# Optimization experiments

Hardware: AMD Instinct MI355X
Metric: run time of the kernel (lower is better)

## Reference

```python
import jax, jax.numpy as jnp
import numpy as np

B, N, F_IN, F_OUT = 8, 2048, 128, 64
ALPHA = 0.2  # LeakyReLU negative slope
NEG_INF = -9e15


def setup_inputs() -> dict:
    key = jax.random.key(0)
    k1, k2, k3, k4 = jax.random.split(key, 4)
    h = jax.random.normal(k1, (B, N, F_IN), dtype=jnp.float32)
    adj = jax.random.randint(k2, (B, N, N), 0, 2, dtype=jnp.int32)
    # xavier_uniform with gain=1.414 approximated by scaled normals (values are arbitrary params)
    W = jax.random.normal(k3, (F_IN, F_OUT), dtype=jnp.float32) * (1.414 * np.sqrt(2.0 / (F_IN + F_OUT)))
    a = jax.random.normal(k4, (2 * F_OUT, 1), dtype=jnp.float32) * (1.414 * np.sqrt(2.0 / (2 * F_OUT + 1)))
    return {"h": h, "adj": adj, "W": W, "a": a}


def reference(h, adj, W, a):
    # Wh: [B, N, F_out]
    Wh = jnp.einsum('bnf,fo->bno', h, W)
    Fo = W.shape[1]
    a1 = a[:Fo, 0]   # [F_out]
    a2 = a[Fo:, 0]   # [F_out]
    # e[b,i,j] = leakyrelu(Wh[b,i]@a1 + Wh[b,j]@a2)  (== cat(Wh_i,Wh_j)@a, same math, no N^2*2F blowup)
    e1 = jnp.einsum('bno,o->bn', Wh, a1)  # [B, N]
    e2 = jnp.einsum('bno,o->bn', Wh, a2)  # [B, N]
    e = e1[:, :, None] + e2[:, None, :]   # [B, N, N]
    e = jnp.where(e > 0, e, ALPHA * e)    # LeakyReLU
    e = jnp.where(adj > 0, e, NEG_INF)    # mask non-edges
    attention = jax.nn.softmax(e, axis=-1)
    # dropout is identity in inference mode (deterministic reference)
    h_prime = jnp.einsum('bij,bjo->bio', attention, Wh)  # [B, N, F_out]
    return jax.nn.elu(h_prime)  # concat=True branch
```

## Files before the change

### kernel.cpp

```cpp
#include <hip/hip_runtime.h>
#include <hip/hip_bf16.h>

#define BB 8
#define NN 2048
#define FIN 128
#define FO 64
#define ALPHA 0.2f

typedef __attribute__((ext_vector_type(8))) short bf16x8;
typedef __attribute__((ext_vector_type(4))) float f32x4;
typedef __attribute__((ext_vector_type(4))) int i32x4;

typedef __attribute__((address_space(1))) const void gvoid;
typedef __attribute__((address_space(3))) void lvoid;

__device__ inline void gl_lds16(const void* g, void* l) {
    __builtin_amdgcn_global_load_lds((gvoid*)g, (lvoid*)l, 16, 0, 0);
}

__device__ inline short f2bf(float x) {
    unsigned u = __float_as_uint(x);
    u += 0x7fffu + ((u >> 16) & 1u);
    return (short)(u >> 16);
}

__global__ __launch_bounds__(256) void wh_kernel(
    const float* __restrict__ h, const float* __restrict__ W,
    const float* __restrict__ a, float* __restrict__ e1, float* __restrict__ e2,
    float* __restrict__ e2p, short* __restrict__ whF)
{
    const int t  = threadIdx.x;
    const int o  = t & 63;
    const int wv = t >> 6;
    const int r0 = blockIdx.x * 32;
    const float* __restrict__ hrow =
        h + (size_t)(r0 + __builtin_amdgcn_readfirstlane(wv) * 8) * FIN;

    float acc[8];
#pragma unroll
    for (int rr = 0; rr < 8; rr++) acc[rr] = 0.f;

    for (int f = 0; f < FIN; f += 4) {
        const float w0 = W[(f + 0) * FO + o];
        const float w1 = W[(f + 1) * FO + o];
        const float w2 = W[(f + 2) * FO + o];
        const float w3 = W[(f + 3) * FO + o];
#pragma unroll
        for (int rr = 0; rr < 8; rr++) {
            const float4 hv = *(const float4*)(hrow + rr * FIN + f);
            acc[rr] = fmaf(hv.x, w0, acc[rr]);
            acc[rr] = fmaf(hv.y, w1, acc[rr]);
            acc[rr] = fmaf(hv.z, w2, acc[rr]);
            acc[rr] = fmaf(hv.w, w3, acc[rr]);
        }
    }

    const int b   = r0 / NN;
    const int ib0 = r0 - b * NN;
    const int ibb = ib0 + wv * 8;
    const int jc  = ibb >> 5;
    const int qq  = (ibb >> 3) & 3;
    const int ot  = o >> 4, mm = o & 15;
    const int L   = mm + qq * 16;
    bf16x8 frag;
#pragma unroll
    for (int rr = 0; rr < 8; rr++) frag[rr] = f2bf(acc[rr]);
    *(bf16x8*)(whF + ((((size_t)(b * 64 + jc) * 4 + ot) * 64 + L) * 8)) = frag;

    const float a1 = a[o], a2 = a[FO + o];
    float vmax = -3.0e38f;
#pragma unroll
    for (int rr = 0; rr < 8; rr++) {
        float v1 = acc[rr] * a1, v2 = acc[rr] * a2;
#pragma unroll
        for (int msk = 32; msk >= 1; msk >>= 1) {
            v1 += __shfl_xor(v1, msk, 64);
            v2 += __shfl_xor(v2, msk, 64);
        }
        vmax = fmaxf(vmax, v2);
        if (o == 0) { e1[r0 + wv * 8 + rr] = v1; e2[r0 + wv * 8 + rr] = v2; }
    }
    if (o == 0) e2p[b * 256 + (ib0 >> 5) * 4 + wv] = vmax;
}

struct SMemS { int adj[2][16][260]; };
struct SMemC { float comb[4][16][64]; float lsum[4][16]; };
union __align__(16) SMemU { SMemS s; SMemC c; };

__global__ __launch_bounds__(256, 4) void attn_kernel(
    const int* __restrict__ adj, const float* __restrict__ e1,
    const float* __restrict__ e2, const float* __restrict__ e2p,
    const short* __restrict__ whF, float* __restrict__ out)
{
    __shared__ SMemU sm;
    __shared__ float red4[4];
    const int t = threadIdx.x, w = t >> 6, lane = t & 63;
    const int m = lane & 15, q = lane >> 4;
    const int blk = blockIdx.x;
    const int b  = blk >> 7;
    const int i0 = (blk & 127) * 16;
    const int i  = i0 + m;

    float pv = e2p[b * 256 + t];
    const float e1v = e1[b * NN + i];
#pragma unroll
    for (int k = 32; k >= 1; k >>= 1) pv = fmaxf(pv, __shfl_xor(pv, k, 64));
    if (lane == 0) red4[w] = pv;
    __syncthreads();
    const float e2mx = fmaxf(fmaxf(red4[0], red4[1]), fmaxf(red4[2], red4[3]));

    float mi = e1v + e2mx;
    mi = mi > 0.f ? mi : ALPHA * mi;

    const short* whFb = whF + (size_t)b * (64 * 4 * 64 * 8);
    const int* arow0 = adj + ((size_t)(b * NN + i0)) * NN + lane * 4;
    const float* e2b = e2 + b * NN;

    f32x4 acc0 = {0.f,0.f,0.f,0.f}, acc1 = acc0, acc2 = acc0, acc3 = acc0;
    float lsum = 0.f;

#pragma unroll
    for (int k = 0; k < 4; k++)
        gl_lds16(arow0 + (size_t)(w * 4 + k) * NN, &sm.s.adj[0][w * 4 + k][0]);

#pragma unroll 2
    for (int tt = 0; tt < 8; tt++) {
        const int j0 = tt * 256;
        const int cb = tt & 1;

        const short* bfpA = whFb + (size_t)((j0 + w * 64) >> 5) * 2048 + lane * 8;
        bf16x8 b00 = *(const bf16x8*)(bfpA);
        bf16x8 b01 = *(const bf16x8*)(bfpA + 512);
        bf16x8 b02 = *(const bf16x8*)(bfpA + 1024);
        bf16x8 b03 = *(const bf16x8*)(bfpA + 1536);
        const short* bfpB = bfpA + 2048;
        bf16x8 b10 = *(const bf16x8*)(bfpB);
        bf16x8 b11 = *(const bf16x8*)(bfpB + 512);
        bf16x8 b12 = *(const bf16x8*)(bfpB + 1024);
        bf16x8 b13 = *(const bf16x8*)(bfpB + 1536);

        const float* e2w = e2b + j0 + w * 64 + q * 8;
        f32x4 ev00 = *(const f32x4*)(e2w);
        f32x4 ev01 = *(const f32x4*)(e2w + 4);
        f32x4 ev10 = *(const f32x4*)(e2w + 32);
        f32x4 ev11 = *(const f32x4*)(e2w + 36);

        asm volatile("" ::: "memory");

        if (tt < 7) {
            const int jn = j0 + 256;
#pragma unroll
            for (int k = 0; k < 4; k++)
                gl_lds16(arow0 + (size_t)(w * 4 + k) * NN + jn,
                         &sm.s.adj[cb ^ 1][w * 4 + k][0]);
            asm volatile("s_waitcnt vmcnt(16)" ::: "memory");
        } else {
            asm volatile("s_waitcnt vmcnt(12)" ::: "memory");
        }
        __builtin_amdgcn_s_barrier();

#pragma unroll
        for (int s2 = 0; s2 < 2; s2++) {
            const int col = w * 64 + s2 * 32 + q * 8;
            i32x4 a0 = *(const i32x4*)&sm.s.adj[cb][m][col];
            i32x4 a1 = *(const i32x4*)&sm.s.adj[cb][m][col + 4];
            const f32x4 ev0 = s2 ? ev10 : ev00;
            const f32x4 ev1 = s2 ? ev11 : ev01;

            bf16x8 af;
#pragma unroll
            for (int jj = 0; jj < 8; jj++) {
                const int   av  = (jj < 4) ? a0[jj]  : a1[jj - 4];
                const float e2j = (jj < 4) ? ev0[jj] : ev1[jj - 4];
                float e = e1v + e2j;
                e = e > 0.f ? e : ALPHA * e;
                const float pe = (av > 0) ? __expf(e - mi) : 0.f;
                lsum += pe;
                af[jj] = f2bf(pe);
            }

            if (s2 == 0) {
                acc0 = __builtin_amdgcn_mfma_f32_16x16x32_bf16(af, b00, acc0, 0, 0, 0);
                acc1 = __builtin_amdgcn_mfma_f32_16x16x32_bf16(af, b01, acc1, 0, 0, 0);
                acc2 = __builtin_amdgcn_mfma_f32_16x16x32_bf16(af, b02, acc2, 0, 0, 0);
                acc3 = __builtin_amdgcn_mfma_f32_16x16x32_bf16(af, b03, acc3, 0, 0, 0);
            } else {
                acc0 = __builtin_amdgcn_mfma_f32_16x16x32_bf16(af, b10, acc0, 0, 0, 0);
                acc1 = __builtin_amdgcn_mfma_f32_16x16x32_bf16(af, b11, acc1, 0, 0, 0);
                acc2 = __builtin_amdgcn_mfma_f32_16x16x32_bf16(af, b12, acc2, 0, 0, 0);
                acc3 = __builtin_amdgcn_mfma_f32_16x16x32_bf16(af, b13, acc3, 0, 0, 0);
            }
        }
        asm volatile("s_waitcnt lgkmcnt(0)" ::: "memory");
        __builtin_amdgcn_s_barrier();
    }

    lsum += __shfl_xor(lsum, 16, 64);
    lsum += __shfl_xor(lsum, 32, 64);
    if (q == 0) sm.c.lsum[w][m] = lsum;
#pragma unroll
    for (int ot = 0; ot < 4; ot++) {
        f32x4 av = (ot == 0) ? acc0 : (ot == 1) ? acc1 : (ot == 2) ? acc2 : acc3;
#pragma unroll
        for (int reg = 0; reg < 4; reg++)
            sm.c.comb[w][q * 4 + reg][ot * 16 + m] = av[reg];
    }
    __syncthreads();

    const int row = t >> 4, c0 = (t & 15) * 4;
    f32x4 sum = *(const f32x4*)&sm.c.comb[0][row][c0];
#pragma unroll
    for (int ww = 1; ww < 4; ww++) {
        f32x4 sv = *(const f32x4*)&sm.c.comb[ww][row][c0];
        sum.x += sv.x; sum.y += sv.y; sum.z += sv.z; sum.w += sv.w;
    }
    float l = sm.c.lsum[0][row] + sm.c.lsum[1][row] + sm.c.lsum[2][row] + sm.c.lsum[3][row];
    l = fmaxf(l, 1e-30f);
    const float rl = 1.f / l;
    float vr[4] = { sum.x * rl, sum.y * rl, sum.z * rl, sum.w * rl };
    f32x4 res;
#pragma unroll
    for (int kk = 0; kk < 4; kk++)
        res[kk] = vr[kk] > 0.f ? vr[kk] : (__expf(vr[kk]) - 1.f);
    *(f32x4*)&out[((size_t)(b * NN + i0 + row)) * FO + c0] = res;
}

extern "C" void kernel_launch(void* const* d_in, const int* in_sizes, int n_in,
                              void* d_out, int out_size, void* d_ws, size_t ws_size,
                              hipStream_t stream) {
    const float* h   = (const float*)d_in[0];
    const int*   adj = (const int*)d_in[1];
    const float* W   = (const float*)d_in[2];
    const float* a   = (const float*)d_in[3];
    float* out = (float*)d_out;

    char* ws = (char*)d_ws;
    short* whF = (short*)ws;
    size_t off = (size_t)BB * 64 * 4 * 64 * 8 * sizeof(short);
    float* e1  = (float*)(ws + off);  off += (size_t)BB * NN * 4;
    float* e2  = (float*)(ws + off);  off += (size_t)BB * NN * 4;
    float* e2p = (float*)(ws + off);

    wh_kernel<<<(BB * NN) / 32, 256, 0, stream>>>(h, W, a, e1, e2, e2p, whF);
    attn_kernel<<<BB * (NN / 16), 256, 0, stream>>>(adj, e1, e2, e2p, whF, out);
}
```

Before: 222.1 us.

## Load adjacency directly to registers, drop LDS staging and per-tile barriers

Replaces the double-buffered global_load_lds staging of adjacency tiles with direct per-lane 32-byte global loads into registers, prefetched one step ahead in a fully unrolled 16-step loop. This removes the LDS round-trip, the manual vmcnt waits and the two barriers per tile, and shrinks shared memory so more blocks can be resident. The cost is that each lane now reads 32-byte segments scattered across 16 rows instead of contiguous rows, which may coalesce less well on a bandwidth-bound adjacency stream. It also raises register pressure from the full unroll.

```diff
diff --git a/kernel.cpp b/kernel.cpp
--- a/kernel.cpp
+++ b/kernel.cpp
@@ -10,13 +10,6 @@
 typedef __attribute__((ext_vector_type(8))) short bf16x8;
 typedef __attribute__((ext_vector_type(4))) float f32x4;
 typedef __attribute__((ext_vector_type(4))) int i32x4;
-
-typedef __attribute__((address_space(1))) const void gvoid;
-typedef __attribute__((address_space(3))) void lvoid;
-
-__device__ inline void gl_lds16(const void* g, void* l) {
-    __builtin_amdgcn_global_load_lds((gvoid*)g, (lvoid*)l, 16, 0, 0);
-}
 
 __device__ inline short f2bf(float x) {
     unsigned u = __float_as_uint(x);
@@ -83,17 +76,41 @@
     if (o == 0) e2p[b * 256 + (ib0 >> 5) * 4 + wv] = vmax;
 }
 
-struct SMemS { int adj[2][16][260]; };
-struct SMemC { float comb[4][16][64]; float lsum[4][16]; };
-union __align__(16) SMemU { SMemS s; SMemC c; };
+struct SMemC { float comb[4][16][64]; float lsum[4][16]; float red4[4]; };
+
+#define STEP(K, A0, A1) do {                                                  \
+    const int sb = ((K) >> 1) * 256 + ((K) & 1) * 32;                         \
+    const short* bfp = whFb + (size_t)((sb + w * 64) >> 5) * 2048 + lane * 8; \
+    bf16x8 b0 = *(const bf16x8*)(bfp);                                        \
+    bf16x8 b1 = *(const bf16x8*)(bfp + 512);                                  \
+    bf16x8 b2 = *(const bf16x8*)(bfp + 1024);                                 \
+    bf16x8 b3 = *(const bf16x8*)(bfp + 1536);                                 \
+    const float* e2w = e2b + sb + w * 64 + q * 8;                             \
+    f32x4 ev0 = *(const f32x4*)(e2w);                                         \
+    f32x4 ev1 = *(const f32x4*)(e2w + 4);                                     \
+    bf16x8 af;                                                                \
+    _Pragma("unroll")                                                         \
+    for (int jj = 0; jj < 8; jj++) {                                          \
+        const int   av  = (jj < 4) ? (A0)[jj] : (A1)[jj - 4];                 \
+        const float e2j = (jj < 4) ? ev0[jj]  : ev1[jj - 4];                  \
+        float e = e1v + e2j;                                                  \
+        e = e > 0.f ? e : ALPHA * e;                                          \
+        const float pe = (av > 0) ? __expf(e - mi) : 0.f;                     \
+        lsum += pe;                                                           \
+        af[jj] = f2bf(pe);                                                    \
+    }                                                                         \
+    acc0 = __builtin_amdgcn_mfma_f32_16x16x32_bf16(af, b0, acc0, 0, 0, 0);    \
+    acc1 = __builtin_amdgcn_mfma_f32_16x16x32_bf16(af, b1, acc1, 0, 0, 0);    \
+    acc2 = __builtin_amdgcn_mfma_f32_16x16x32_bf16(af, b2, acc2, 0, 0, 0);    \
+    acc3 = __builtin_amdgcn_mfma_f32_16x16x32_bf16(af, b3, acc3, 0, 0, 0);    \
+} while (0)
 
 __global__ __launch_bounds__(256, 4) void attn_kernel(
     const int* __restrict__ adj, const float* __restrict__ e1,
     const float* __restrict__ e2, const float* __restrict__ e2p,
     const short* __restrict__ whF, float* __restrict__ out)
 {
-    __shared__ SMemU sm;
-    __shared__ float red4[4];
+    __shared__ SMemC sm;
     const int t = threadIdx.x, w = t >> 6, lane = t & 63;
     const int m = lane & 15, q = lane >> 4;
     const int blk = blockIdx.x;
@@ -105,116 +122,53 @@
     const float e1v = e1[b * NN + i];
 #pragma unroll
     for (int k = 32; k >= 1; k >>= 1) pv = fmaxf(pv, __shfl_xor(pv, k, 64));
-    if (lane == 0) red4[w] = pv;
+    if (lane == 0) sm.red4[w] = pv;
     __syncthreads();
-    const float e2mx = fmaxf(fmaxf(red4[0], red4[1]), fmaxf(red4[2], red4[3]));
+    const float e2mx = fmaxf(fmaxf(sm.red4[0], sm.red4[1]),
+                             fmaxf(sm.red4[2], sm.red4[3]));
 
     float mi = e1v + e2mx;
     mi = mi > 0.f ? mi : ALPHA * mi;
 
     const short* whFb = whF + (size_t)b * (64 * 4 * 64 * 8);
-    const int* arow0 = adj + ((size_t)(b * NN + i0)) * NN + lane * 4;
+    const int* arow = adj + ((size_t)(b * NN + i)) * NN + w * 64 + q * 8;
     const float* e2b = e2 + b * NN;
 
     f32x4 acc0 = {0.f,0.f,0.f,0.f}, acc1 = acc0, acc2 = acc0, acc3 = acc0;
     float lsum = 0.f;
 
-#pragma unroll
-    for (int k = 0; k < 4; k++)
-        gl_lds16(arow0 + (size_t)(w * 4 + k) * NN, &sm.s.adj[0][w * 4 + k][0]);
-
-#pragma unroll 2
-    for (int tt = 0; tt < 8; tt++) {
-        const int j0 = tt * 256;
-        const int cb = tt & 1;
-
-        const short* bfpA = whFb + (size_t)((j0 + w * 64) >> 5) * 2048 + lane * 8;
-        bf16x8 b00 = *(const bf16x8*)(bfpA);
-        bf16x8 b01 = *(const bf16x8*)(bfpA + 512);
-        bf16x8 b02 = *(const bf16x8*)(bfpA + 1024);
-        bf16x8 b03 = *(const bf16x8*)(bfpA + 1536);
-        const short* bfpB = bfpA + 2048;
-        bf16x8 b10 = *(const bf16x8*)(bfpB);
-        bf16x8 b11 = *(const bf16x8*)(bfpB + 512);
-        bf16x8 b12 = *(const bf16x8*)(bfpB + 1024);
-        bf16x8 b13 = *(const bf16x8*)(bfpB + 1536);
-
-        const float* e2w = e2b + j0 + w * 64 + q * 8;
-        f32x4 ev00 = *(const f32x4*)(e2w);
-        f32x4 ev01 = *(const f32x4*)(e2w + 4);
-        f32x4 ev10 = *(const f32x4*)(e2w + 32);
-        f32x4 ev11 = *(const f32x4*)(e2w + 36);
-
-        asm volatile("" ::: "memory");
-
-        if (tt < 7) {
-            const int jn = j0 + 256;
-#pragma unroll
-            for (int k = 0; k < 4; k++)
-                gl_lds16(arow0 + (size_t)(w * 4 + k) * NN + jn,
-                         &sm.s.adj[cb ^ 1][w * 4 + k][0]);
-            asm volatile("s_waitcnt vmcnt(16)" ::: "memory");
-        } else {
-            asm volatile("s_waitcnt vmcnt(12)" ::: "memory");
-        }
-        __builtin_amdgcn_s_barrier();
-
-#pragma unroll
-        for (int s2 = 0; s2 < 2; s2++) {
-            const int col = w * 64 + s2 * 32 + q * 8;
-            i32x4 a0 = *(const i32x4*)&sm.s.adj[cb][m][col];
-            i32x4 a1 = *(const i32x4*)&sm.s.adj[cb][m][col + 4];
-            const f32x4 ev0 = s2 ? ev10 : ev00;
-            const f32x4 ev1 = s2 ? ev11 : ev01;
-
-            bf16x8 af;
-#pragma unroll
-            for (int jj = 0; jj < 8; jj++) {
-                const int   av  = (jj < 4) ? a0[jj]  : a1[jj - 4];
-                const float e2j = (jj < 4) ? ev0[jj] : ev1[jj - 4];
-                float e = e1v + e2j;
-                e = e > 0.f ? e : ALPHA * e;
-                const float pe = (av > 0) ? __expf(e - mi) : 0.f;
-                lsum += pe;
-                af[jj] = f2bf(pe);
-            }
-
-            if (s2 == 0) {
-                acc0 = __builtin_amdgcn_mfma_f32_16x16x32_bf16(af, b00, acc0, 0, 0, 0);
-                acc1 = __builtin_amdgcn_mfma_f32_16x16x32_bf16(af, b01, acc1, 0, 0, 0);
-                acc2 = __builtin_amdgcn_mfma_f32_16x16x32_bf16(af, b02, acc2, 0, 0, 0);
-                acc3 = __builtin_amdgcn_mfma_f32_16x16x32_bf16(af, b03, acc3, 0, 0, 0);
-            } else {
-                acc0 = __builtin_amdgcn_mfma_f32_16x16x32_bf16(af, b10, acc0, 0, 0, 0);
-                acc1 = __builtin_amdgcn_mfma_f32_16x16x32_bf16(af, b11, acc1, 0, 0, 0);
-                acc2 = __builtin_amdgcn_mfma_f32_16x16x32_bf16(af, b12, acc2, 0, 0, 0);
-                acc3 = __builtin_amdgcn_mfma_f32_16x16x32_bf16(af, b13, acc3, 0, 0, 0);
-            }
-        }
-        asm volatile("s_waitcnt lgkmcnt(0)" ::: "memory");
-        __builtin_amdgcn_s_barrier();
-    }
+    i32x4 ca0 = *(const i32x4*)(arow);
+    i32x4 ca1 = *(const i32x4*)(arow + 4);
+#pragma unroll
+    for (int k = 0; k < 15; k++) {
+        const int nsb = ((k + 1) >> 1) * 256 + ((k + 1) & 1) * 32;
+        i32x4 na0 = *(const i32x4*)(arow + nsb);
+        i32x4 na1 = *(const i32x4*)(arow + nsb + 4);
+        STEP(k, ca0, ca1);
+        ca0 = na0; ca1 = na1;
+    }
+    STEP(15, ca0, ca1);
 
     lsum += __shfl_xor(lsum, 16, 64);
     lsum += __shfl_xor(lsum, 32, 64);
-    if (q == 0) sm.c.lsum[w][m] = lsum;
+    if (q == 0) sm.lsum[w][m] = lsum;
 #pragma unroll
     for (int ot = 0; ot < 4; ot++) {
         f32x4 av = (ot == 0) ? acc0 : (ot == 1) ? acc1 : (ot == 2) ? acc2 : acc3;
 #pragma unroll
         for (int reg = 0; reg < 4; reg++)
-            sm.c.comb[w][q * 4 + reg][ot * 16 + m] = av[reg];
+            sm.comb[w][q * 4 + reg][ot * 16 + m] = av[reg];
     }
     __syncthreads();
 
     const int row = t >> 4, c0 = (t & 15) * 4;
-    f32x4 sum = *(const f32x4*)&sm.c.comb[0][row][c0];
+    f32x4 sum = *(const f32x4*)&sm.comb[0][row][c0];
 #pragma unroll
     for (int ww = 1; ww < 4; ww++) {
-        f32x4 sv = *(const f32x4*)&sm.c.comb[ww][row][c0];
+        f32x4 sv = *(const f32x4*)&sm.comb[ww][row][c0];
         sum.x += sv.x; sum.y += sv.y; sum.z += sv.z; sum.w += sv.w;
     }
-    float l = sm.c.lsum[0][row] + sm.c.lsum[1][row] + sm.c.lsum[2][row] + sm.c.lsum[3][row];
+    float l = sm.lsum[0][row] + sm.lsum[1][row] + sm.lsum[2][row] + sm.lsum[3][row];
     l = fmaxf(l, 1e-30f);
     const float rl = 1.f / l;
     float vr[4] = { sum.x * rl, sum.y * rl, sum.z * rl, sum.w * rl };
```

New measurement: 266.1 us. 19.8% more time.
